# Performance work log

Measured on AMD Instinct MI355X. Metric: run time of the kernel, lower is better.

The kernel has to match this reference:

```python
import jax, jax.numpy as jnp
import numpy as np

B, N, D = 64, 2048, 64
KC = 512
BETA = 0.5


def setup_inputs() -> dict:
    key = jax.random.key(0)
    k1, k2, k3 = jax.random.split(key, 3)
    F_active = jax.random.normal(k1, (B, N, D), dtype=jnp.float32)
    centers = jax.random.normal(k2, (KC, D), dtype=jnp.float32)
    psi = 0.1 * jax.random.normal(k3, (KC,), dtype=jnp.float32)
    beta = jnp.float32(BETA)
    return {"F_active": F_active, "centers": centers, "psi": psi, "beta": beta}


def reference(F_active, centers, psi, beta):
    # Squared Euclidean distance via GEMM expansion (avoids the (B,N,Kc,d) diff tensor):
    # ||f - c||^2 = ||f||^2 + ||c||^2 - 2 f.c
    f2 = jnp.sum(F_active * F_active, axis=-1, keepdims=True)          # (B, N, 1)
    c2 = jnp.sum(centers * centers, axis=-1)                           # (Kc,)
    fc = jnp.einsum('bnd,kd->bnk', F_active, centers)                  # (B, N, Kc)
    dist2 = jnp.maximum(f2 + c2[None, None, :] - 2.0 * fc, 0.0)       # (B, N, Kc)
    sim = jnp.exp(-beta * dist2)                                       # (B, N, Kc)
    w = jax.nn.softmax(psi, axis=0)                                    # (Kc,)
    score_per_slot = jnp.einsum('bnk,k->bn', sim, w)                   # (B, N)
    return jnp.mean(score_per_slot, axis=1)                            # (B,)
```

## Files before the change

### kernel.cpp

```cpp
#include <hip/hip_runtime.h>

typedef _Float16 f16x8 __attribute__((ext_vector_type(8)));
typedef float f32x4 __attribute__((ext_vector_type(4)));

static constexpr float kLog2e = 1.44269504088896340736f;

#define WS_EW 65536

__device__ __forceinline__ float fast_exp2(float x) {
#if __has_builtin(__builtin_amdgcn_exp2f)
  return __builtin_amdgcn_exp2f(x);
#else
  return exp2f(x);
#endif
}

__global__ __launch_bounds__(64) void prep_kernel(
    const float* __restrict__ centers, const float* __restrict__ psi,
    const float* __restrict__ beta, _Float16* __restrict__ cfrag,
    float2* __restrict__ ew, float* __restrict__ out) {
  const int tid = threadIdx.x;
  const int c = blockIdx.x * 64 + tid;
  const float b = beta[0];
  const float kco = -b * kLog2e;

  float4 row[16];
  const float4* crow = (const float4*)(centers + c * 64);
  float c2 = 0.f;
#pragma unroll
  for (int i = 0; i < 16; ++i) {
    row[i] = crow[i];
    c2 = fmaf(row[i].x, row[i].x, c2); c2 = fmaf(row[i].y, row[i].y, c2);
    c2 = fmaf(row[i].z, row[i].z, c2); c2 = fmaf(row[i].w, row[i].w, c2);
  }

  const float4 pv0 = *(const float4*)(psi + tid * 8);
  const float4 pv1 = *(const float4*)(psi + tid * 8 + 4);
  float m = fmaxf(fmaxf(fmaxf(pv0.x, pv0.y), fmaxf(pv0.z, pv0.w)),
                  fmaxf(fmaxf(pv1.x, pv1.y), fmaxf(pv1.z, pv1.w)));
#pragma unroll
  for (int d = 1; d < 64; d <<= 1) m = fmaxf(m, __shfl_xor(m, d, 64));
  float ls = fast_exp2((pv0.x - m) * kLog2e) + fast_exp2((pv0.y - m) * kLog2e) +
             fast_exp2((pv0.z - m) * kLog2e) + fast_exp2((pv0.w - m) * kLog2e) +
             fast_exp2((pv1.x - m) * kLog2e) + fast_exp2((pv1.y - m) * kLog2e) +
             fast_exp2((pv1.z - m) * kLog2e) + fast_exp2((pv1.w - m) * kLog2e);
#pragma unroll
  for (int d = 1; d < 64; d <<= 1) ls += __shfl_xor(ls, d, 64);
  const float ex = fast_exp2((psi[c] - m) * kLog2e);
  ew[c] = make_float2(kco * c2, ex / ls);

  const int t = c >> 4;
  const int l15 = c & 15;
#pragma unroll
  for (int kk = 0; kk < 2; ++kk) {
#pragma unroll
    for (int quad = 0; quad < 4; ++quad) {
      const int idx = (t * 2 + kk) * 64 + quad * 16 + l15;
      const float4 v0 = row[kk * 8 + quad * 2];
      const float4 v1 = row[kk * 8 + quad * 2 + 1];
      f16x8 h;
      h[0] = (_Float16)v0.x; h[1] = (_Float16)v0.y;
      h[2] = (_Float16)v0.z; h[3] = (_Float16)v0.w;
      h[4] = (_Float16)v1.x; h[5] = (_Float16)v1.y;
      h[6] = (_Float16)v1.z; h[7] = (_Float16)v1.w;
      *(f16x8*)(cfrag + (size_t)idx * 8) = h;
    }
  }

  if (blockIdx.x == 0) out[tid] = 0.f;
}

__global__ __launch_bounds__(512, 4) void score_kernel(
    const float* __restrict__ F, const _Float16* __restrict__ cfrag,
    const float2* __restrict__ ew, const float* __restrict__ beta,
    float* __restrict__ out) {
  __shared__ float wsum[8];
  const int tid = threadIdx.x;
  const int lane = tid & 63;
  const int wv = tid >> 6;
  const int rg = wv >> 2;
  const int wr = wv & 3;
  const int quad = lane >> 4;
  const int l15 = lane & 15;
  const int R0 = blockIdx.x * 256;

  const float b = beta[0];
  const float cC = 2.f * b * kLog2e;
  const float kco = -b * kLog2e;

  f16x8 a[4][2];
  float ssqv[4];
#pragma unroll
  for (int rt = 0; rt < 4; ++rt) {
    const int row = R0 + wr * 64 + rt * 16 + l15;
    const float* fr = F + row * 64 + quad * 8;
    float ssq = 0.f;
#pragma unroll
    for (int kk = 0; kk < 2; ++kk) {
      const float4 v0 = *(const float4*)(fr + kk * 32);
      const float4 v1 = *(const float4*)(fr + kk * 32 + 4);
      ssq = fmaf(v0.x, v0.x, ssq); ssq = fmaf(v0.y, v0.y, ssq);
      ssq = fmaf(v0.z, v0.z, ssq); ssq = fmaf(v0.w, v0.w, ssq);
      ssq = fmaf(v1.x, v1.x, ssq); ssq = fmaf(v1.y, v1.y, ssq);
      ssq = fmaf(v1.z, v1.z, ssq); ssq = fmaf(v1.w, v1.w, ssq);
      a[rt][kk][0] = (_Float16)(cC * v0.x); a[rt][kk][1] = (_Float16)(cC * v0.y);
      a[rt][kk][2] = (_Float16)(cC * v0.z); a[rt][kk][3] = (_Float16)(cC * v0.w);
      a[rt][kk][4] = (_Float16)(cC * v1.x); a[rt][kk][5] = (_Float16)(cC * v1.y);
      a[rt][kk][6] = (_Float16)(cC * v1.z); a[rt][kk][7] = (_Float16)(cC * v1.w);
    }
    ssq += __shfl_xor(ssq, 16, 64);
    ssq += __shfl_xor(ssq, 32, 64);
    ssqv[rt] = ssq;
  }

  float p0[4][4];
#pragma unroll
  for (int rt = 0; rt < 4; ++rt)
#pragma unroll
    for (int r = 0; r < 4; ++r)
      p0[rt][r] = kco * __shfl(ssqv[rt], quad * 4 + r, 64);

  float s = 0.f;
  const int tbase = rg * 16;
#pragma unroll 2
  for (int ti = 0; ti < 16; ++ti) {
    const int t = tbase + ti;
    const f16x8 b0 = *(const f16x8*)(cfrag + (size_t)((t * 2 + 0) * 64 + lane) * 8);
    const f16x8 b1 = *(const f16x8*)(cfrag + (size_t)((t * 2 + 1) * 64 + lane) * 8);
    const float2 ewv = ew[t * 16 + l15];
    float esum = 0.f;
#pragma unroll
    for (int rt = 0; rt < 4; ++rt) {
      f32x4 acc = {p0[rt][0] + ewv.x, p0[rt][1] + ewv.x,
                   p0[rt][2] + ewv.x, p0[rt][3] + ewv.x};
      acc = __builtin_amdgcn_mfma_f32_16x16x32_f16(a[rt][0], b0, acc, 0, 0, 0);
      acc = __builtin_amdgcn_mfma_f32_16x16x32_f16(a[rt][1], b1, acc, 0, 0, 0);
#pragma unroll
      for (int r = 0; r < 4; ++r)
        esum += fast_exp2(fminf(acc[r], 0.f));
    }
    s = fmaf(ewv.y, esum, s);
  }

#pragma unroll
  for (int d = 1; d < 64; d <<= 1) s += __shfl_xor(s, d, 64);
  if (lane == 0) wsum[wv] = s;
  __syncthreads();
  if (tid == 0) {
    float tot = 0.f;
#pragma unroll
    for (int i = 0; i < 8; ++i) tot += wsum[i];
    atomicAdd(out + (blockIdx.x >> 3), tot * (1.0f / 2048.0f));
  }
}

extern "C" void kernel_launch(void* const* d_in, const int* in_sizes, int n_in,
                              void* d_out, int out_size, void* d_ws, size_t ws_size,
                              hipStream_t stream) {
  const float* F = (const float*)d_in[0];
  const float* centers = (const float*)d_in[1];
  const float* psi = (const float*)d_in[2];
  const float* beta = (const float*)d_in[3];
  float* out = (float*)d_out;
  char* ws = (char*)d_ws;
  _Float16* cfrag = (_Float16*)ws;
  float2* ew = (float2*)(ws + WS_EW);

  prep_kernel<<<8, 64, 0, stream>>>(centers, psi, beta, cfrag, ew, out);
  score_kernel<<<512, 512, 0, stream>>>(F, cfrag, ew, beta, out);
}
```

Measured before the change: 97.73 us.

## Fuse center preprocessing into score kernel via LDS and replace atomics with finalize

Removes the separate prep kernel: each score block converts all 512 centers to fp16 MFMA fragments in shared memory and computes the psi softmax weights and center norms itself. The inner loop then reads B fragments from LDS instead of global memory. Per-block partial sums go to a workspace and a small finalize kernel reduces them, replacing the atomicAdd and the output zeroing. The cost is redundant preprocessing in every block, extra barriers, and 66KB of LDS per block, which limits occupancy.

```diff
diff --git a/kernel.cpp b/kernel.cpp
--- a/kernel.cpp
+++ b/kernel.cpp
@@ -4,8 +4,6 @@
 typedef float f32x4 __attribute__((ext_vector_type(4)));
 
 static constexpr float kLog2e = 1.44269504088896340736f;
-
-#define WS_EW 65536
 
 __device__ __forceinline__ float fast_exp2(float x) {
 #if __has_builtin(__builtin_amdgcn_exp2f)
@@ -15,66 +13,15 @@
 #endif
 }
 
-__global__ __launch_bounds__(64) void prep_kernel(
-    const float* __restrict__ centers, const float* __restrict__ psi,
-    const float* __restrict__ beta, _Float16* __restrict__ cfrag,
-    float2* __restrict__ ew, float* __restrict__ out) {
-  const int tid = threadIdx.x;
-  const int c = blockIdx.x * 64 + tid;
-  const float b = beta[0];
-  const float kco = -b * kLog2e;
+__global__ __launch_bounds__(512, 4) void score_kernel(
+    const float* __restrict__ F, const float* __restrict__ centers,
+    const float* __restrict__ psi, const float* __restrict__ beta,
+    float* __restrict__ ws) {
+  __shared__ _Float16 cfrag[32768];
+  __shared__ float2 ewl[512];
+  __shared__ float red[8];
+  __shared__ float wsum[8];
 
-  float4 row[16];
-  const float4* crow = (const float4*)(centers + c * 64);
-  float c2 = 0.f;
-#pragma unroll
-  for (int i = 0; i < 16; ++i) {
-    row[i] = crow[i];
-    c2 = fmaf(row[i].x, row[i].x, c2); c2 = fmaf(row[i].y, row[i].y, c2);
-    c2 = fmaf(row[i].z, row[i].z, c2); c2 = fmaf(row[i].w, row[i].w, c2);
-  }
-
-  const float4 pv0 = *(const float4*)(psi + tid * 8);
-  const float4 pv1 = *(const float4*)(psi + tid * 8 + 4);
-  float m = fmaxf(fmaxf(fmaxf(pv0.x, pv0.y), fmaxf(pv0.z, pv0.w)),
-                  fmaxf(fmaxf(pv1.x, pv1.y), fmaxf(pv1.z, pv1.w)));
-#pragma unroll
-  for (int d = 1; d < 64; d <<= 1) m = fmaxf(m, __shfl_xor(m, d, 64));
-  float ls = fast_exp2((pv0.x - m) * kLog2e) + fast_exp2((pv0.y - m) * kLog2e) +
-             fast_exp2((pv0.z - m) * kLog2e) + fast_exp2((pv0.w - m) * kLog2e) +
-             fast_exp2((pv1.x - m) * kLog2e) + fast_exp2((pv1.y - m) * kLog2e) +
-             fast_exp2((pv1.z - m) * kLog2e) + fast_exp2((pv1.w - m) * kLog2e);
-#pragma unroll
-  for (int d = 1; d < 64; d <<= 1) ls += __shfl_xor(ls, d, 64);
-  const float ex = fast_exp2((psi[c] - m) * kLog2e);
-  ew[c] = make_float2(kco * c2, ex / ls);
-
-  const int t = c >> 4;
-  const int l15 = c & 15;
-#pragma unroll
-  for (int kk = 0; kk < 2; ++kk) {
-#pragma unroll
-    for (int quad = 0; quad < 4; ++quad) {
-      const int idx = (t * 2 + kk) * 64 + quad * 16 + l15;
-      const float4 v0 = row[kk * 8 + quad * 2];
-      const float4 v1 = row[kk * 8 + quad * 2 + 1];
-      f16x8 h;
-      h[0] = (_Float16)v0.x; h[1] = (_Float16)v0.y;
-      h[2] = (_Float16)v0.z; h[3] = (_Float16)v0.w;
-      h[4] = (_Float16)v1.x; h[5] = (_Float16)v1.y;
-      h[6] = (_Float16)v1.z; h[7] = (_Float16)v1.w;
-      *(f16x8*)(cfrag + (size_t)idx * 8) = h;
-    }
-  }
-
-  if (blockIdx.x == 0) out[tid] = 0.f;
-}
-
-__global__ __launch_bounds__(512, 4) void score_kernel(
-    const float* __restrict__ F, const _Float16* __restrict__ cfrag,
-    const float2* __restrict__ ew, const float* __restrict__ beta,
-    float* __restrict__ out) {
-  __shared__ float wsum[8];
   const int tid = threadIdx.x;
   const int lane = tid & 63;
   const int wv = tid >> 6;
@@ -87,6 +34,54 @@
   const float b = beta[0];
   const float cC = 2.f * b * kLog2e;
   const float kco = -b * kLog2e;
+
+  {
+    const int c = tid;
+    const int t = c >> 4;
+    const int cl = c & 15;
+    const float4* crow = (const float4*)(centers + c * 64);
+    float c2 = 0.f;
+#pragma unroll
+    for (int kk = 0; kk < 2; ++kk) {
+#pragma unroll
+      for (int q = 0; q < 4; ++q) {
+        const float4 v0 = crow[kk * 8 + q * 2];
+        const float4 v1 = crow[kk * 8 + q * 2 + 1];
+        c2 = fmaf(v0.x, v0.x, c2); c2 = fmaf(v0.y, v0.y, c2);
+        c2 = fmaf(v0.z, v0.z, c2); c2 = fmaf(v0.w, v0.w, c2);
+        c2 = fmaf(v1.x, v1.x, c2); c2 = fmaf(v1.y, v1.y, c2);
+        c2 = fmaf(v1.z, v1.z, c2); c2 = fmaf(v1.w, v1.w, c2);
+        f16x8 h;
+        h[0] = (_Float16)v0.x; h[1] = (_Float16)v0.y;
+        h[2] = (_Float16)v0.z; h[3] = (_Float16)v0.w;
+        h[4] = (_Float16)v1.x; h[5] = (_Float16)v1.y;
+        h[6] = (_Float16)v1.z; h[7] = (_Float16)v1.w;
+        const int idx = (t * 2 + kk) * 64 + q * 16 + cl;
+        *(f16x8*)(cfrag + idx * 8) = h;
+      }
+    }
+    const float p = psi[c];
+    float m = p;
+#pragma unroll
+    for (int d = 1; d < 64; d <<= 1) m = fmaxf(m, __shfl_xor(m, d, 64));
+    if (lane == 0) red[wv] = m;
+    __syncthreads();
+    float mx = red[0];
+#pragma unroll
+    for (int i = 1; i < 8; ++i) mx = fmaxf(mx, red[i]);
+    __syncthreads();
+    const float ex = fast_exp2((p - mx) * kLog2e);
+    float ss = ex;
+#pragma unroll
+    for (int d = 1; d < 64; d <<= 1) ss += __shfl_xor(ss, d, 64);
+    if (lane == 0) red[wv] = ss;
+    __syncthreads();
+    float tot = 0.f;
+#pragma unroll
+    for (int i = 0; i < 8; ++i) tot += red[i];
+    ewl[c] = make_float2(kco * c2, ex / tot);
+  }
+  __syncthreads();
 
   f16x8 a[4][2];
   float ssqv[4];
@@ -125,9 +120,9 @@
 #pragma unroll 2
   for (int ti = 0; ti < 16; ++ti) {
     const int t = tbase + ti;
-    const f16x8 b0 = *(const f16x8*)(cfrag + (size_t)((t * 2 + 0) * 64 + lane) * 8);
-    const f16x8 b1 = *(const f16x8*)(cfrag + (size_t)((t * 2 + 1) * 64 + lane) * 8);
-    const float2 ewv = ew[t * 16 + l15];
+    const f16x8 b0 = *(const f16x8*)(cfrag + ((t * 2 + 0) * 64 + lane) * 8);
+    const f16x8 b1 = *(const f16x8*)(cfrag + ((t * 2 + 1) * 64 + lane) * 8);
+    const float2 ewv = ewl[t * 16 + l15];
     float esum = 0.f;
 #pragma unroll
     for (int rt = 0; rt < 4; ++rt) {
@@ -150,8 +145,17 @@
     float tot = 0.f;
 #pragma unroll
     for (int i = 0; i < 8; ++i) tot += wsum[i];
-    atomicAdd(out + (blockIdx.x >> 3), tot * (1.0f / 2048.0f));
+    ws[blockIdx.x] = tot;
   }
+}
+
+__global__ __launch_bounds__(64) void finalize_kernel(
+    const float* __restrict__ ws, float* __restrict__ out) {
+  const int b = threadIdx.x;
+  float t = 0.f;
+#pragma unroll
+  for (int j = 0; j < 8; ++j) t += ws[b * 8 + j];
+  out[b] = t * (1.0f / 2048.0f);
 }
 
 extern "C" void kernel_launch(void* const* d_in, const int* in_sizes, int n_in,
@@ -162,10 +166,8 @@
   const float* psi = (const float*)d_in[2];
   const float* beta = (const float*)d_in[3];
   float* out = (float*)d_out;
-  char* ws = (char*)d_ws;
-  _Float16* cfrag = (_Float16*)ws;
-  float2* ew = (float2*)(ws + WS_EW);
+  float* ws = (float*)d_ws;
 
-  prep_kernel<<<8, 64, 0, stream>>>(centers, psi, beta, cfrag, ew, out);
-  score_kernel<<<512, 512, 0, stream>>>(F, cfrag, ew, beta, out);
+  score_kernel<<<512, 512, 0, stream>>>(F, centers, psi, beta, ws);
+  finalize_kernel<<<1, 64, 0, stream>>>(ws, out);
 }
```

Result: no change. 99.40 us (+1.7%).
